# Kernel optimization log

Measured on AMD Instinct MI355X. Metric: run time of the kernel, lower is better.

The kernel has to match this reference:

```python
import math
import jax, jax.numpy as jnp
import numpy as np

N_KINDS = 8
D_MODEL = 256
B_FEAT = 24  # Fourier bands; MLP input dim is 2*B_FEAT
SIGMA = 8.0


def setup_inputs() -> dict:
    key = jax.random.key(0)
    ks = jax.random.split(key, 8)
    N, S = 32, 2048
    values = jax.random.normal(ks[0], (N, S, 1), dtype=jnp.float32)
    kinds = jax.random.randint(ks[1], (N, S), 0, N_KINDS, dtype=jnp.int32)
    # Frozen Fourier projection matrix (torch: randn(in_dim, B) * sigma, requires_grad=False)
    Bmat = jax.random.normal(ks[2], (1, B_FEAT), dtype=jnp.float32) * SIGMA
    # Kind embedding table
    kind_emb = jax.random.normal(ks[3], (N_KINDS, D_MODEL), dtype=jnp.float32) * 0.02
    # Per-kind two-layer MLP params
    W1 = jax.random.normal(ks[4], (N_KINDS, 2 * B_FEAT, D_MODEL), dtype=jnp.float32) / math.sqrt(2 * B_FEAT)
    b1 = jnp.zeros((N_KINDS, D_MODEL), dtype=jnp.float32)
    W2 = jax.random.normal(ks[5], (N_KINDS, D_MODEL, D_MODEL), dtype=jnp.float32) / math.sqrt(D_MODEL)
    b2 = jnp.zeros((N_KINDS, D_MODEL), dtype=jnp.float32)
    return {"values": values, "kinds": kinds, "Bmat": Bmat,
            "kind_emb": kind_emb, "W1": W1, "b1": b1, "W2": W2, "b2": b2}


def reference(values, kinds, Bmat, kind_emb, W1, b1, W2, b2):
    N, S, _ = values.shape
    T = N * S
    d = kind_emb.shape[-1]
    # Fourier features: [T, 2B]
    y = (2.0 * math.pi) * values.reshape(T, 1) @ Bmat  # [T, B]
    ff = jnp.concatenate([jnp.sin(y), jnp.cos(y)], axis=-1)  # [T, 2B]
    kinds_flat = kinds.reshape(T)
    out = jnp.zeros((T, d), dtype=values.dtype)
    # kinds partition the tokens, so masked combine == the torch scatter-assign
    for k in range(kind_emb.shape[0]):
        h = jax.nn.gelu(ff @ W1[k] + b1[k], approximate=False)  # torch GELU is exact erf
        o = h @ W2[k] + b2[k]  # [T, d]
        out = jnp.where((kinds_flat == k)[:, None], o, out)
    return out.reshape(N, S, d) + kind_emb[kinds]
```

## Files before the change

### kernel.cpp

```cpp
#include <hip/hip_runtime.h>
#include <hip/hip_bf16.h>
#include <math.h>


#define NK 8
#define DM 256
#define TMAX 65536
#define NBLK 256
#define W1PK 16384
#define W2PK 65536
#define LDSTRIDE 262

typedef __attribute__((ext_vector_type(8))) short   s16x8;
typedef __attribute__((ext_vector_type(8))) __bf16  bf16x8;
typedef __attribute__((ext_vector_type(4))) float   f32x4;
typedef __attribute__((ext_vector_type(2))) float   f32x2;
typedef __attribute__((ext_vector_type(4))) int     i32x4;

__device__ int   g_counts[NK];
__device__ __align__(16) int g_blkcnt[NBLK][NK];
__device__ int   g_bucket[(size_t)NK * TMAX];
__device__ __align__(16) short g_W1p[(size_t)NK * W1PK];
__device__ __align__(16) short g_W2p[(size_t)NK * W2PK];

static __device__ __forceinline__ short f2bf(float f) {
    __hip_bfloat16 h = __float2bfloat16(f);
    return __builtin_bit_cast(short, h);
}

static __device__ __forceinline__ f32x4 mfma16(s16x8 a, s16x8 b, f32x4 c) {
    return __builtin_amdgcn_mfma_f32_16x16x32_bf16(
        __builtin_bit_cast(bf16x8, a), __builtin_bit_cast(bf16x8, b), c, 0, 0, 0);
}

__global__ __launch_bounds__(256) void prep_kernel(const float* __restrict__ W1,
                                                   const float* __restrict__ W2,
                                                   const int* __restrict__ kinds, int T) {
    __shared__ float ld[32 * LDSTRIDE];
    __shared__ int wcnt[4][NK];
    const int tid = threadIdx.x;
    const int bid = blockIdx.x;
    if (bid < 80) {
        const int isW1 = (bid >= 64);
        int kind, kt;
        if (isW1) { kind = (bid - 64) >> 1; kt = (bid - 64) & 1; }
        else      { kind = bid >> 3;        kt = bid & 7; }
        #pragma unroll
        for (int i = 0; i < 8; ++i) {
            int f = tid + i * 256;
            int row = f >> 6, col = (f & 63) * 4;
            int kk = kt * 32 + row;
            f32x4 v = (f32x4){0.f, 0.f, 0.f, 0.f};
            if (isW1) {
                if (kk < 48) v = *(const f32x4*)(W1 + ((size_t)kind * 48 + kk) * DM + col);
            } else {
                v = *(const f32x4*)(W2 + ((size_t)kind * DM + kk) * DM + col);
            }
            float* dst = &ld[row * LDSTRIDE + col];
            *(f32x2*)dst       = (f32x2){v[0], v[1]};
            *(f32x2*)(dst + 2) = (f32x2){v[2], v[3]};
        }
        __syncthreads();
        short* outp = isW1 ? (g_W1p + (size_t)kind * W1PK) : (g_W2p + (size_t)kind * W2PK);
        #pragma unroll
        for (int i = 0; i < 4; ++i) {
            int g = tid + i * 256;
            int ntile = g >> 6, l = g & 63;
            int kk0 = (l >> 4) * 8, n = ntile * 16 + (l & 15);
            s16x8 v;
            #pragma unroll
            for (int j = 0; j < 8; ++j) v[j] = f2bf(ld[(kk0 + j) * LDSTRIDE + n]);
            *(s16x8*)(outp + ((size_t)(kt * 16 + ntile) * 64 + l) * 8) = v;
        }
    } else {
        const int b = bid - 80;
        const int wave = tid >> 6, lane = tid & 63;
        int t = b * 256 + tid;
        int k = (t < T) ? kinds[t] : -1;
        #pragma unroll
        for (int kk = 0; kk < NK; ++kk) {
            unsigned long long m = __ballot(k == kk);
            if (lane == 0) wcnt[wave][kk] = __popcll(m);
        }
        __syncthreads();
        if (tid < NK) {
            int s = 0;
            #pragma unroll
            for (int w = 0; w < 4; ++w) s += wcnt[w][tid];
            g_blkcnt[b][tid] = s;
        }
    }
}

__global__ __launch_bounds__(256) void scatter_kernel(const int* __restrict__ kinds, int T) {
    __shared__ int cnt_s[NBLK * NK];
    __shared__ int wcnt[4][NK];
    __shared__ int base_s[NK];
    const int tid = threadIdx.x, wave = tid >> 6, lane = tid & 63;
    const int b = blockIdx.x;
    {
        const i32x4* src = (const i32x4*)&g_blkcnt[0][0];
        i32x4* dst = (i32x4*)cnt_s;
        dst[tid]       = src[tid];
        dst[tid + 256] = src[tid + 256];
    }
    int t = b * 256 + tid;
    int k = (t < T) ? kinds[t] : -1;
    int rank = 0;
    #pragma unroll
    for (int kk = 0; kk < NK; ++kk) {
        unsigned long long m = __ballot(k == kk);
        if (lane == 0) wcnt[wave][kk] = __popcll(m);
        if (k == kk) rank = __popcll(m & ((1ull << lane) - 1ull));
    }
    __syncthreads();
    if (tid < NK) {
        int s = 0;
        for (int bb = 0; bb < NBLK; ++bb) {
            if (bb == b) base_s[tid] = s;
            s += cnt_s[bb * NK + tid];
        }
        if (b == 0) g_counts[tid] = s;
        int ws = 0;
        #pragma unroll
        for (int w = 0; w < 4; ++w) { int c = wcnt[w][tid]; wcnt[w][tid] = ws; ws += c; }
    }
    __syncthreads();
    if (k >= 0)
        g_bucket[(size_t)k * T + base_s[k] + wcnt[wave][k] + rank] = t;
}

__global__ __launch_bounds__(256, 4) void fproj_gemm(
    const float* __restrict__ values, const float* __restrict__ Bmat,
    const float* __restrict__ kind_emb, const float* __restrict__ b1,
    const float* __restrict__ b2, float* __restrict__ out, int T)
{
    int cnts[NK];
    #pragma unroll
    for (int i = 0; i < NK; ++i) cnts[i] = g_counts[i];
    const int bid = blockIdx.x;
    int k = -1, m0 = 0, cum = 0, cnt = 0;
    #pragma unroll
    for (int kk = 0; kk < NK; ++kk) {
        int tk = (cnts[kk] + 63) >> 6;
        if (k < 0 && bid < cum + tk) { k = kk; m0 = (bid - cum) * 64; cnt = cnts[kk]; }
        cum += tk;
    }
    if (k < 0) return;
    const int valid = min(64, cnt - m0);

    __shared__ short Hpack[16384];
    __shared__ int   toks[64];
    __shared__ float vals[64];
    short* Apack = Hpack;

    const int tid  = threadIdx.x;
    const int wave = tid >> 6;
    const int lane = tid & 63;
    const int quad = lane >> 4;
    const int cl   = lane & 15;

    const s16x8* B1p = (const s16x8*)(g_W1p + (size_t)k * W1PK);
    s16x8 b1f[2][4];
    #pragma unroll
    for (int kt = 0; kt < 2; ++kt)
        #pragma unroll
        for (int nt = 0; nt < 4; ++nt)
            b1f[kt][nt] = B1p[(kt * 16 + wave * 4 + nt) * 64 + lane];

    if (tid < 64) {
        int t = -1; float v = 0.0f;
        if (tid < valid) { t = g_bucket[(size_t)k * T + m0 + tid]; v = values[t]; }
        toks[tid] = t; vals[tid] = v;
    }
    __syncthreads();

    for (int idx = tid; idx < 4096; idx += 256) {
        int m = idx >> 6, kk = idx & 63;
        float f = 0.0f;
        if (kk < 48) {
            int b = (kk < 24) ? kk : kk - 24;
            float y = 6.283185307179586f * vals[m] * Bmat[b];
            f = (kk < 24) ? __sinf(y) : __cosf(y);
        }
        int mt = m >> 4, kt = kk >> 5, q = (kk >> 3) & 3, j = kk & 7;
        int l = (m & 15) | (q << 4);
        Apack[((kt * 4 + mt) << 9) + (l << 3) + j] = f2bf(f);
    }
    __syncthreads();

    f32x4 acc[4][4];
    #pragma unroll
    for (int mt = 0; mt < 4; ++mt)
        #pragma unroll
        for (int nt = 0; nt < 4; ++nt) acc[mt][nt] = (f32x4){0.f, 0.f, 0.f, 0.f};

    const s16x8* Ap = (const s16x8*)Apack;
    #pragma unroll
    for (int kt = 0; kt < 2; ++kt) {
        s16x8 a[4];
        #pragma unroll
        for (int mt = 0; mt < 4; ++mt) a[mt] = Ap[(kt * 4 + mt) * 64 + lane];
        #pragma unroll
        for (int mt = 0; mt < 4; ++mt)
            #pragma unroll
            for (int nt = 0; nt < 4; ++nt) acc[mt][nt] = mfma16(a[mt], b1f[kt][nt], acc[mt][nt]);
    }
    __syncthreads();

    #pragma unroll
    for (int nt = 0; nt < 4; ++nt) {
        int c = wave * 64 + nt * 16 + cl;
        float bias = b1[k * DM + c];
        int kt2 = c >> 5, q2 = (c >> 3) & 3, j2 = c & 7;
        #pragma unroll
        for (int mt = 0; mt < 4; ++mt)
            #pragma unroll
            for (int r4 = 0; r4 < 4; ++r4) {
                int r = mt * 16 + quad * 4 + r4;
                float x = acc[mt][nt][r4] + bias;
                float h = 0.5f * x * (1.0f + erff(x * 0.7071067811865476f));
                int l2 = (r & 15) | (q2 << 4);
                Hpack[((kt2 * 4 + (r >> 4)) << 9) + (l2 << 3) + j2] = f2bf(h);
            }
    }
    __syncthreads();

    float addc[4];
    #pragma unroll
    for (int nt = 0; nt < 4; ++nt) {
        int c = wave * 64 + nt * 16 + cl;
        addc[nt] = b2[k * DM + c] + kind_emb[k * DM + c];
    }

    f32x4 acc2[4][4];
    #pragma unroll
    for (int mt = 0; mt < 4; ++mt)
        #pragma unroll
        for (int nt = 0; nt < 4; ++nt) acc2[mt][nt] = (f32x4){0.f, 0.f, 0.f, 0.f};

    const s16x8* Hp  = (const s16x8*)Hpack;
    const s16x8* B2p = (const s16x8*)(g_W2p + (size_t)k * W2PK);
    #pragma unroll
    for (int kt = 0; kt < 8; ++kt) {
        s16x8 a[4], b[4];
        #pragma unroll
        for (int mt = 0; mt < 4; ++mt) a[mt] = Hp[(kt * 4 + mt) * 64 + lane];
        #pragma unroll
        for (int nt = 0; nt < 4; ++nt) b[nt] = B2p[(kt * 16 + wave * 4 + nt) * 64 + lane];
        #pragma unroll
        for (int mt = 0; mt < 4; ++mt)
            #pragma unroll
            for (int nt = 0; nt < 4; ++nt) acc2[mt][nt] = mfma16(a[mt], b[nt], acc2[mt][nt]);
    }

    #pragma unroll
    for (int nt = 0; nt < 4; ++nt) {
        int c = wave * 64 + nt * 16 + cl;
        #pragma unroll
        for (int mt = 0; mt < 4; ++mt)
            #pragma unroll
            for (int r4 = 0; r4 < 4; ++r4) {
                int r = mt * 16 + quad * 4 + r4;
                if (r < valid)
                    __builtin_nontemporal_store(acc2[mt][nt][r4] + addc[nt],
                                                out + (size_t)toks[r] * DM + c);
            }
    }
}

extern "C" void kernel_launch(void* const* d_in, const int* in_sizes, int n_in,
                              void* d_out, int out_size, void* d_ws, size_t ws_size,
                              hipStream_t stream) {
    const float* values   = (const float*)d_in[0];
    const int*   kinds    = (const int*)  d_in[1];
    const float* Bmat     = (const float*)d_in[2];
    const float* kind_emb = (const float*)d_in[3];
    const float* W1       = (const float*)d_in[4];
    const float* b1       = (const float*)d_in[5];
    const float* W2       = (const float*)d_in[6];
    const float* b2       = (const float*)d_in[7];
    float* out = (float*)d_out;
    const int T = in_sizes[0];

    prep_kernel<<<dim3(80 + NBLK), dim3(256), 0, stream>>>(W1, W2, kinds, T);
    scatter_kernel<<<dim3(NBLK), dim3(256), 0, stream>>>(kinds, T);
    fproj_gemm<<<dim3(T / 64 + NK), dim3(256), 0, stream>>>(values, Bmat, kind_emb,
                                                            b1, b2, out, T);
}
```

Before: 143.7 us.

## Halve GEMM row tile, prefetch W2 fragments, use sigmoid GELU approximation

Row tile per block drops from 64 to 32 tokens, which doubles the grid and halves LDS and accumulator use. Token and value gathers go straight to the bucket in global memory instead of through shared staging, which removes one barrier. W2 fragments are double-buffered across k-steps, and exact erf GELU is replaced with a tanh-style sigmoid approximation. The smaller tile means W2 is reloaded twice as often per token, and the GELU approximation changes numerics.

```diff
diff --git a/kernel.cpp b/kernel.cpp
--- a/kernel.cpp
+++ b/kernel.cpp
@@ -31,6 +31,14 @@
 static __device__ __forceinline__ f32x4 mfma16(s16x8 a, s16x8 b, f32x4 c) {
     return __builtin_amdgcn_mfma_f32_16x16x32_bf16(
         __builtin_bit_cast(bf16x8, a), __builtin_bit_cast(bf16x8, b), c, 0, 0, 0);
+}
+
+static __device__ __forceinline__ float gelu_fast(float x) {
+    float t1 = x * x;
+    float m  = fmaf(0.0713548162726f, t1, 1.59576912161f);
+    float z  = m * x;
+    float e  = __expf(-z);
+    return x * __frcp_rn(1.0f + e);
 }
 
 __global__ __launch_bounds__(256) void prep_kernel(const float* __restrict__ W1,
@@ -142,16 +150,15 @@
     int k = -1, m0 = 0, cum = 0, cnt = 0;
     #pragma unroll
     for (int kk = 0; kk < NK; ++kk) {
-        int tk = (cnts[kk] + 63) >> 6;
-        if (k < 0 && bid < cum + tk) { k = kk; m0 = (bid - cum) * 64; cnt = cnts[kk]; }
+        int tk = (cnts[kk] + 31) >> 5;
+        if (k < 0 && bid < cum + tk) { k = kk; m0 = (bid - cum) * 32; cnt = cnts[kk]; }
         cum += tk;
     }
     if (k < 0) return;
-    const int valid = min(64, cnt - m0);
-
-    __shared__ short Hpack[16384];
-    __shared__ int   toks[64];
-    __shared__ float vals[64];
+    const int valid = min(32, cnt - m0);
+    const int* buck = g_bucket + (size_t)k * T + m0;
+
+    __shared__ short Hpack[8192];
     short* Apack = Hpack;
 
     const int tid  = threadIdx.x;
@@ -168,41 +175,38 @@
         for (int nt = 0; nt < 4; ++nt)
             b1f[kt][nt] = B1p[(kt * 16 + wave * 4 + nt) * 64 + lane];
 
-    if (tid < 64) {
-        int t = -1; float v = 0.0f;
-        if (tid < valid) { t = g_bucket[(size_t)k * T + m0 + tid]; v = values[t]; }
-        toks[tid] = t; vals[tid] = v;
-    }
-    __syncthreads();
-
-    for (int idx = tid; idx < 4096; idx += 256) {
+    #pragma unroll
+    for (int i = 0; i < 8; ++i) {
+        int idx = tid + i * 256;
         int m = idx >> 6, kk = idx & 63;
         float f = 0.0f;
         if (kk < 48) {
+            float v = 0.0f;
+            if (m < valid) v = values[buck[m]];
             int b = (kk < 24) ? kk : kk - 24;
-            float y = 6.283185307179586f * vals[m] * Bmat[b];
+            float y = 6.283185307179586f * v * Bmat[b];
             f = (kk < 24) ? __sinf(y) : __cosf(y);
         }
         int mt = m >> 4, kt = kk >> 5, q = (kk >> 3) & 3, j = kk & 7;
         int l = (m & 15) | (q << 4);
-        Apack[((kt * 4 + mt) << 9) + (l << 3) + j] = f2bf(f);
-    }
-    __syncthreads();
-
-    f32x4 acc[4][4];
-    #pragma unroll
-    for (int mt = 0; mt < 4; ++mt)
+        Apack[((kt * 2 + mt) << 9) + (l << 3) + j] = f2bf(f);
+    }
+    __syncthreads();
+
+    f32x4 acc[2][4];
+    #pragma unroll
+    for (int mt = 0; mt < 2; ++mt)
         #pragma unroll
         for (int nt = 0; nt < 4; ++nt) acc[mt][nt] = (f32x4){0.f, 0.f, 0.f, 0.f};
 
     const s16x8* Ap = (const s16x8*)Apack;
     #pragma unroll
     for (int kt = 0; kt < 2; ++kt) {
-        s16x8 a[4];
-        #pragma unroll
-        for (int mt = 0; mt < 4; ++mt) a[mt] = Ap[(kt * 4 + mt) * 64 + lane];
-        #pragma unroll
-        for (int mt = 0; mt < 4; ++mt)
+        s16x8 a[2];
+        #pragma unroll
+        for (int mt = 0; mt < 2; ++mt) a[mt] = Ap[(kt * 2 + mt) * 64 + lane];
+        #pragma unroll
+        for (int mt = 0; mt < 2; ++mt)
             #pragma unroll
             for (int nt = 0; nt < 4; ++nt) acc[mt][nt] = mfma16(a[mt], b1f[kt][nt], acc[mt][nt]);
     }
@@ -214,14 +218,13 @@
         float bias = b1[k * DM + c];
         int kt2 = c >> 5, q2 = (c >> 3) & 3, j2 = c & 7;
         #pragma unroll
-        for (int mt = 0; mt < 4; ++mt)
+        for (int mt = 0; mt < 2; ++mt)
             #pragma unroll
             for (int r4 = 0; r4 < 4; ++r4) {
                 int r = mt * 16 + quad * 4 + r4;
-                float x = acc[mt][nt][r4] + bias;
-                float h = 0.5f * x * (1.0f + erff(x * 0.7071067811865476f));
+                float h = gelu_fast(acc[mt][nt][r4] + bias);
                 int l2 = (r & 15) | (q2 << 4);
-                Hpack[((kt2 * 4 + (r >> 4)) << 9) + (l2 << 3) + j2] = f2bf(h);
+                Hpack[((kt2 * 2 + mt) << 9) + (l2 << 3) + j2] = f2bf(h);
             }
     }
     __syncthreads();
@@ -233,40 +236,49 @@
         addc[nt] = b2[k * DM + c] + kind_emb[k * DM + c];
     }
 
-    f32x4 acc2[4][4];
-    #pragma unroll
-    for (int mt = 0; mt < 4; ++mt)
+    f32x4 acc2[2][4];
+    #pragma unroll
+    for (int mt = 0; mt < 2; ++mt)
         #pragma unroll
         for (int nt = 0; nt < 4; ++nt) acc2[mt][nt] = (f32x4){0.f, 0.f, 0.f, 0.f};
 
     const s16x8* Hp  = (const s16x8*)Hpack;
     const s16x8* B2p = (const s16x8*)(g_W2p + (size_t)k * W2PK);
+    s16x8 bcur[4], bnxt[4];
+    #pragma unroll
+    for (int nt = 0; nt < 4; ++nt) bcur[nt] = B2p[(wave * 4 + nt) * 64 + lane];
     #pragma unroll
     for (int kt = 0; kt < 8; ++kt) {
-        s16x8 a[4], b[4];
-        #pragma unroll
-        for (int mt = 0; mt < 4; ++mt) a[mt] = Hp[(kt * 4 + mt) * 64 + lane];
-        #pragma unroll
-        for (int nt = 0; nt < 4; ++nt) b[nt] = B2p[(kt * 16 + wave * 4 + nt) * 64 + lane];
-        #pragma unroll
-        for (int mt = 0; mt < 4; ++mt)
-            #pragma unroll
-            for (int nt = 0; nt < 4; ++nt) acc2[mt][nt] = mfma16(a[mt], b[nt], acc2[mt][nt]);
-    }
-
-    #pragma unroll
-    for (int nt = 0; nt < 4; ++nt) {
-        int c = wave * 64 + nt * 16 + cl;
-        #pragma unroll
-        for (int mt = 0; mt < 4; ++mt)
-            #pragma unroll
-            for (int r4 = 0; r4 < 4; ++r4) {
-                int r = mt * 16 + quad * 4 + r4;
-                if (r < valid)
-                    __builtin_nontemporal_store(acc2[mt][nt][r4] + addc[nt],
-                                                out + (size_t)toks[r] * DM + c);
+        if (kt < 7) {
+            #pragma unroll
+            for (int nt = 0; nt < 4; ++nt)
+                bnxt[nt] = B2p[((kt + 1) * 16 + wave * 4 + nt) * 64 + lane];
+        }
+        s16x8 a[2];
+        #pragma unroll
+        for (int mt = 0; mt < 2; ++mt) a[mt] = Hp[(kt * 2 + mt) * 64 + lane];
+        #pragma unroll
+        for (int mt = 0; mt < 2; ++mt)
+            #pragma unroll
+            for (int nt = 0; nt < 4; ++nt) acc2[mt][nt] = mfma16(a[mt], bcur[nt], acc2[mt][nt]);
+        #pragma unroll
+        for (int nt = 0; nt < 4; ++nt) bcur[nt] = bnxt[nt];
+    }
+
+    #pragma unroll
+    for (int mt = 0; mt < 2; ++mt)
+        #pragma unroll
+        for (int r4 = 0; r4 < 4; ++r4) {
+            int r = mt * 16 + quad * 4 + r4;
+            if (r < valid) {
+                size_t row = (size_t)buck[r] * DM;
+                #pragma unroll
+                for (int nt = 0; nt < 4; ++nt) {
+                    int c = wave * 64 + nt * 16 + cl;
+                    __builtin_nontemporal_store(acc2[mt][nt][r4] + addc[nt], out + row + c);
+                }
             }
-    }
+        }
 }
 
 extern "C" void kernel_launch(void* const* d_in, const int* in_sizes, int n_in,
@@ -285,6 +297,6 @@
 
     prep_kernel<<<dim3(80 + NBLK), dim3(256), 0, stream>>>(W1, W2, kinds, T);
     scatter_kernel<<<dim3(NBLK), dim3(256), 0, stream>>>(kinds, T);
-    fproj_gemm<<<dim3(T / 64 + NK), dim3(256), 0, stream>>>(values, Bmat, kind_emb,
+    fproj_gemm<<<dim3(T / 32 + NK), dim3(256), 0, stream>>>(values, Bmat, kind_emb,
                                                             b1, b2, out, T);
 }
```

Result: faster. 127.9 us (-11.0%).
